# Kernel tuning notes

Measured on AMD Instinct MI355X. Metric: run time of the kernel, lower is better.

Reference implementation:

```python
import jax, jax.numpy as jnp
import numpy as np

B, N, IN_DIM, OUT_DIM = 8, 2048, 128, 128
NEG_SLOPE = 0.2

def setup_inputs() -> dict:
    key = jax.random.key(0)
    k1, k2, k3, k4 = jax.random.split(key, 4)
    x = jax.random.normal(k1, (B, N, IN_DIM), dtype=jnp.float32)
    adj = jax.random.randint(k2, (N, N), 0, 2, dtype=jnp.int32)
    # nn.Linear weight init scale ~ 1/sqrt(fan_in)
    W = jax.random.normal(k3, (IN_DIM, OUT_DIM), dtype=jnp.float32) / np.sqrt(IN_DIM)
    a_vec = jax.random.normal(k4, (2 * OUT_DIM,), dtype=jnp.float32) / np.sqrt(2 * OUT_DIM)
    return {"x": x, "adj": adj, "W": W, "a_vec": a_vec}

def reference(x, adj, W, a_vec):
    # h = x @ W : [b, n, d]
    h = jnp.einsum("bni,io->bno", x, W)
    # Algebraic decomposition of a([h_i, h_j]) = a1.h_i + a2.h_j
    a1, a2 = a_vec[:OUT_DIM], a_vec[OUT_DIM:]
    s_i = h @ a1  # [b, n] score contribution from source node i
    s_j = h @ a2  # [b, n] score contribution from target node j
    e = s_i[:, :, None] + s_j[:, None, :]  # [b, n, n]
    e = jnp.where(e >= 0, e, NEG_SLOPE * e)  # leaky_relu(0.2)
    mask = (adj > 0)[None, :, :]  # [1, n, n] broadcast over batch
    e = jnp.where(mask, e, -jnp.inf)
    alpha = jax.nn.softmax(e, axis=-1)  # [b, n, n]
    out = jnp.einsum("bnm,bmd->bnd", alpha, h)  # [b, n, d]
    return out, alpha
```

## Files before the change

kernel.cpp:

```cpp
#include <hip/hip_runtime.h>
#include <hip/hip_bf16.h>
#include <cstdint>
#include <cstddef>

constexpr int Bn = 8;
constexpr int Nn = 2048;
constexpr int Dn = 128;

typedef __bf16 bf16x8 __attribute__((ext_vector_type(8)));
typedef float f32x4 __attribute__((ext_vector_type(4)));

#define AS1 __attribute__((address_space(1)))
#define AS3 __attribute__((address_space(3)))

static __device__ __forceinline__ void gl_lds16(const void* g, void* l) {
  __builtin_amdgcn_global_load_lds((AS1 const void*)g, (AS3 void*)l, 16, 0, 0);
}

__global__ __launch_bounds__(256) void gat_k1(
    const float* __restrict__ x, const float* __restrict__ W,
    const float* __restrict__ a_vec,
    __bf16* __restrict__ hT, float* __restrict__ s1, float* __restrict__ s2) {
  __shared__ __align__(16) float Wl[64 * 144];
  __shared__ __align__(16) float xL[32 * 132];

  const int t = threadIdx.x;
  const int r0 = blockIdx.x * 32;
  const int b = r0 >> 11;
  const int n0 = r0 & (Nn - 1);
  const int rp = (t >> 4) << 1;
  const int c0 = (t & 15) << 3;
  const int c0p = c0 + ((c0 >> 5) << 2);

  float acc[2][8];
#pragma unroll
  for (int r = 0; r < 2; ++r)
#pragma unroll
    for (int c = 0; c < 8; ++c) acc[r][c] = 0.f;

#pragma unroll
  for (int it = 0; it < 4; ++it) {
    int idx = t + (it << 8);
    int rr = idx >> 5, kc = (idx & 31) << 2;
    *(float4*)(xL + rr * 132 + kc) = *(const float4*)(x + (size_t)(r0 + rr) * Dn + kc);
  }

  for (int ph = 0; ph < 2; ++ph) {
    if (ph) __syncthreads();
#pragma unroll
    for (int it = 0; it < 8; ++it) {
      int idx = t + (it << 8);
      int kk = idx >> 5, c4 = (idx & 31) << 2;
      int dsto = kk * 144 + c4 + ((c4 >> 5) << 2);
      *(float4*)(Wl + dsto) = *(const float4*)(W + (size_t)((ph << 6) + kk) * Dn + c4);
    }
    __syncthreads();
    const float* xrow = xL + rp * 132 + (ph << 6);
    for (int k = 0; k < 64; ++k) {
      float xa0 = xrow[k];
      float xa1 = xrow[132 + k];
      float4 w0 = *(const float4*)(Wl + k * 144 + c0p);
      float4 w1 = *(const float4*)(Wl + k * 144 + c0p + 4);
      float ws[8] = {w0.x, w0.y, w0.z, w0.w, w1.x, w1.y, w1.z, w1.w};
#pragma unroll
      for (int c = 0; c < 8; ++c) {
        acc[0][c] = fmaf(xa0, ws[c], acc[0][c]);
        acc[1][c] = fmaf(xa1, ws[c], acc[1][c]);
      }
    }
  }

  float q1[2] = {0.f, 0.f}, q2[2] = {0.f, 0.f};
#pragma unroll
  for (int c = 0; c < 8; ++c) {
    float a1c = a_vec[c0 + c];
    float a2c = a_vec[Dn + c0 + c];
    q1[0] = fmaf(acc[0][c], a1c, q1[0]);
    q1[1] = fmaf(acc[1][c], a1c, q1[1]);
    q2[0] = fmaf(acc[0][c], a2c, q2[0]);
    q2[1] = fmaf(acc[1][c], a2c, q2[1]);
  }
#pragma unroll
  for (int d = 1; d < 16; d <<= 1) {
    q1[0] += __shfl_xor(q1[0], d);
    q1[1] += __shfl_xor(q1[1], d);
    q2[0] += __shfl_xor(q2[0], d);
    q2[1] += __shfl_xor(q2[1], d);
  }
  if ((t & 15) == 0) {
    s1[b * Nn + n0 + rp] = q1[0];
    s1[b * Nn + n0 + rp + 1] = q1[1];
    s2[b * Nn + n0 + rp] = q2[0];
    s2[b * Nn + n0 + rp + 1] = q2[1];
  }

#pragma unroll
  for (int c = 0; c < 8; ++c) {
    union { __bf16 h[2]; uint32_t u; } pk;
    pk.h[0] = (__bf16)acc[0][c];
    pk.h[1] = (__bf16)acc[1][c];
    *(uint32_t*)(hT + (size_t)(b * Dn + c0 + c) * Nn + n0 + rp) = pk.u;
  }
}

__global__ __launch_bounds__(512) void gat_k2(
    const int* __restrict__ adj, const __bf16* __restrict__ hT,
    const float* __restrict__ s1, const float* __restrict__ s2,
    float* __restrict__ out, float* __restrict__ alpha) {
  __shared__ __align__(16) float sj[Nn];
  __shared__ float siv[32], invl[32];
  __shared__ __align__(16) __bf16 Pl[2][32 * 72];
  __shared__ __align__(16) __bf16 hl[3 * 128 * 64];

  const int t = threadIdx.x;
  const int b = blockIdx.x >> 6;
  const int i0 = (blockIdx.x & 63) << 5;
  const int w = t >> 6, lane = t & 63;
  const int ii = t >> 4, sub = t & 15;
  const int lrow = lane >> 3, ccs = lane & 7;
  const __bf16* __restrict__ hTb = hT + (size_t)b * Dn * Nn;

#pragma unroll
  for (int inst = 0; inst < 2; ++inst) {
    int row = (w << 4) + (inst << 3) + lrow;
    gl_lds16(hTb + (size_t)row * Nn + ((ccs ^ lrow) << 3),
             &hl[((w << 4) + (inst << 3)) << 6]);
  }

  *(float4*)(sj + (t << 2)) = *(const float4*)(s2 + b * Nn + (t << 2));
  if (t < 32) siv[t] = s1[b * Nn + i0 + t];
  __syncthreads();

  const int i = i0 + ii;
  const int* __restrict__ adjrow = adj + (size_t)i * Nn;
  const float si = siv[ii];

  float l = 0.f;
  uint32_t mb0 = 0, mb1 = 0, mb2 = 0, mb3 = 0;
#define PASS1_G(G, MW)                                                        \
  {                                                                           \
    _Pragma("unroll")                                                         \
    for (int u = 0; u < 8; ++u) {                                             \
      int j = (((G) << 3) + u) * 64 + (sub << 2);                             \
      int4 am = *(const int4*)(adjrow + j);                                   \
      float4 sv = *(const float4*)(sj + j);                                   \
      float e0 = si + sv.x; e0 = fmaxf(e0, 0.2f * e0);                        \
      float e1 = si + sv.y; e1 = fmaxf(e1, 0.2f * e1);                        \
      float e2 = si + sv.z; e2 = fmaxf(e2, 0.2f * e2);                        \
      float e3 = si + sv.w; e3 = fmaxf(e3, 0.2f * e3);                        \
      l += (am.x > 0) ? __expf(e0) : 0.f;                                     \
      l += (am.y > 0) ? __expf(e1) : 0.f;                                     \
      l += (am.z > 0) ? __expf(e2) : 0.f;                                     \
      l += (am.w > 0) ? __expf(e3) : 0.f;                                     \
      uint32_t mbt = (am.x > 0 ? 1u : 0u) | (am.y > 0 ? 2u : 0u) |            \
                     (am.z > 0 ? 4u : 0u) | (am.w > 0 ? 8u : 0u);             \
      MW |= mbt << (u << 2);                                                  \
    }                                                                         \
  }
  PASS1_G(0, mb0)
  PASS1_G(1, mb1)
  PASS1_G(2, mb2)
  PASS1_G(3, mb3)
#undef PASS1_G

  l += __shfl_xor(l, 1);
  l += __shfl_xor(l, 2);
  l += __shfl_xor(l, 4);
  l += __shfl_xor(l, 8);
  if (sub == 0) invl[ii] = 1.f / l;
  __syncthreads();
  const float il = invl[ii];

  const int iw = (w & 1) << 4;
  const int nd0 = (w >> 1) << 5;
  const int q16 = lane >> 4, m16 = lane & 15;
  f32x4 acc0 = {0.f, 0.f, 0.f, 0.f}, acc1 = {0.f, 0.f, 0.f, 0.f};
  float* __restrict__ arow = alpha + ((size_t)(b * Nn + i) << 11);

  auto alpha_phase = [&](int k, int parity) {
    int j = (k << 6) + (sub << 2);
    float4 sv = *(const float4*)(sj + j);
    uint32_t mw = (k & 16) ? ((k & 8) ? mb3 : mb2) : ((k & 8) ? mb1 : mb0);
    int sh = (k & 7) << 2;
    float e0 = si + sv.x; e0 = fmaxf(e0, 0.2f * e0);
    float e1 = si + sv.y; e1 = fmaxf(e1, 0.2f * e1);
    float e2 = si + sv.z; e2 = fmaxf(e2, 0.2f * e2);
    float e3 = si + sv.w; e3 = fmaxf(e3, 0.2f * e3);
    float a0 = ((mw >> (sh + 0)) & 1u) ? __expf(e0) * il : 0.f;
    float a1 = ((mw >> (sh + 1)) & 1u) ? __expf(e1) * il : 0.f;
    float a2 = ((mw >> (sh + 2)) & 1u) ? __expf(e2) * il : 0.f;
    float a3 = ((mw >> (sh + 3)) & 1u) ? __expf(e3) * il : 0.f;
    f32x4 av = {a0, a1, a2, a3};
    __builtin_nontemporal_store(av, (f32x4*)(arow + j));
    union { __bf16 h[4]; uint2 u2; } pk;
    pk.h[0] = (__bf16)a0; pk.h[1] = (__bf16)a1;
    pk.h[2] = (__bf16)a2; pk.h[3] = (__bf16)a3;
    *(uint2*)(&Pl[parity][ii * 72 + (sub << 2)]) = pk.u2;
  };

  auto mfma_phase = [&](int parity, const __bf16* hb) {
#pragma unroll
    for (int ks = 0; ks < 2; ++ks) {
      bf16x8 af = *(const bf16x8*)(&Pl[parity][(iw + m16) * 72 + (ks << 5) + (q16 << 3)]);
      {
        int d = nd0 + m16;
        int phys = ((ks << 2) + q16) ^ (d & 7);
        bf16x8 bv = *(const bf16x8*)(&hb[(d << 6) + (phys << 3)]);
        acc0 = __builtin_amdgcn_mfma_f32_16x16x32_bf16(af, bv, acc0, 0, 0, 0);
      }
      {
        int d = nd0 + 16 + m16;
        int phys = ((ks << 2) + q16) ^ (d & 7);
        bf16x8 bv = *(const bf16x8*)(&hb[(d << 6) + (phys << 3)]);
        acc1 = __builtin_amdgcn_mfma_f32_16x16x32_bf16(af, bv, acc1, 0, 0, 0);
      }
    }
  };

  auto stage = [&](int jn, int bidx) {
#pragma unroll
    for (int inst = 0; inst < 2; ++inst) {
      int row = (w << 4) + (inst << 3) + lrow;
      gl_lds16(hTb + (size_t)row * Nn + jn + ((ccs ^ lrow) << 3),
               &hl[(bidx << 13) + (((w << 4) + (inst << 3)) << 6)]);
    }
  };

  stage(64, 1);
  __builtin_amdgcn_sched_barrier(0);
  alpha_phase(0, 0);
  asm volatile("s_waitcnt lgkmcnt(0)\n\ts_barrier" ::: "memory");

  int bi = 0;
  for (int jt = 0; jt < 30; ++jt) {
    int bp = bi + 2;
    if (bp >= 3) bp -= 3;
    stage((jt + 2) << 6, bp);
    __builtin_amdgcn_sched_barrier(0);
    mfma_phase(jt & 1, &hl[bi << 13]);
    alpha_phase(jt + 1, (jt + 1) & 1);
    asm volatile("s_waitcnt vmcnt(4) lgkmcnt(0)\n\ts_barrier" ::: "memory");
    bi = (bi == 2) ? 0 : bi + 1;
  }
  mfma_phase(0, &hl[0]);
  alpha_phase(31, 1);
  asm volatile("s_waitcnt vmcnt(2) lgkmcnt(0)\n\ts_barrier" ::: "memory");
  mfma_phase(1, &hl[1 << 13]);

#pragma unroll
  for (int nb = 0; nb < 2; ++nb) {
    f32x4 a = nb ? acc1 : acc0;
    int d = nd0 + (nb << 4) + m16;
#pragma unroll
    for (int r = 0; r < 4; ++r) {
      int irow = i0 + iw + (q16 << 2) + r;
      out[((size_t)(b * Nn + irow) << 7) + d] = a[r];
    }
  }
}

extern "C" void kernel_launch(void* const* d_in, const int* in_sizes, int n_in,
                              void* d_out, int out_size, void* d_ws, size_t ws_size,
                              hipStream_t stream) {
  const float* x = (const float*)d_in[0];
  const int* adj = (const int*)d_in[1];
  const float* W = (const float*)d_in[2];
  const float* a_vec = (const float*)d_in[3];

  float* out = (float*)d_out;
  float* alpha = out + (size_t)Bn * Nn * Dn;

  char* ws = (char*)d_ws;
  __bf16* hT = (__bf16*)ws;
  float* s1 = (float*)(ws + (size_t)Bn * Dn * Nn * 2);
  float* s2 = s1 + (size_t)Bn * Nn;

  gat_k1<<<512, 256, 0, stream>>>(x, W, a_vec, hT, s1, s2);
  gat_k2<<<512, 512, 0, stream>>>(adj, hT, s1, s2, out, alpha);
}
```

Measured before the change: 213.4 us.

## Load hT B-operands directly from global into registers, drop LDS triple buffer

```diff
diff --git a/kernel.cpp b/kernel.cpp
--- a/kernel.cpp
+++ b/kernel.cpp
@@ -9,13 +9,6 @@
 
 typedef __bf16 bf16x8 __attribute__((ext_vector_type(8)));
 typedef float f32x4 __attribute__((ext_vector_type(4)));
-
-#define AS1 __attribute__((address_space(1)))
-#define AS3 __attribute__((address_space(3)))
-
-static __device__ __forceinline__ void gl_lds16(const void* g, void* l) {
-  __builtin_amdgcn_global_load_lds((AS1 const void*)g, (AS3 void*)l, 16, 0, 0);
-}
 
 __global__ __launch_bounds__(256) void gat_k1(
     const float* __restrict__ x, const float* __restrict__ W,
@@ -110,22 +103,15 @@
   __shared__ __align__(16) float sj[Nn];
   __shared__ float siv[32], invl[32];
   __shared__ __align__(16) __bf16 Pl[2][32 * 72];
-  __shared__ __align__(16) __bf16 hl[3 * 128 * 64];
 
   const int t = threadIdx.x;
   const int b = blockIdx.x >> 6;
   const int i0 = (blockIdx.x & 63) << 5;
   const int w = t >> 6, lane = t & 63;
   const int ii = t >> 4, sub = t & 15;
-  const int lrow = lane >> 3, ccs = lane & 7;
+  const int q16 = lane >> 4, m16 = lane & 15;
+  const int d0 = w << 4;
   const __bf16* __restrict__ hTb = hT + (size_t)b * Dn * Nn;
-
-#pragma unroll
-  for (int inst = 0; inst < 2; ++inst) {
-    int row = (w << 4) + (inst << 3) + lrow;
-    gl_lds16(hTb + (size_t)row * Nn + ((ccs ^ lrow) << 3),
-             &hl[((w << 4) + (inst << 3)) << 6]);
-  }
 
   *(float4*)(sj + (t << 2)) = *(const float4*)(s2 + b * Nn + (t << 2));
   if (t < 32) siv[t] = s1[b * Nn + i0 + t];
@@ -171,13 +157,12 @@
   __syncthreads();
   const float il = invl[ii];
 
-  const int iw = (w & 1) << 4;
-  const int nd0 = (w >> 1) << 5;
-  const int q16 = lane >> 4, m16 = lane & 15;
   f32x4 acc0 = {0.f, 0.f, 0.f, 0.f}, acc1 = {0.f, 0.f, 0.f, 0.f};
   float* __restrict__ arow = alpha + ((size_t)(b * Nn + i) << 11);
 
-  auto alpha_phase = [&](int k, int parity) {
+  const __bf16* __restrict__ bp = hTb + (size_t)(d0 + m16) * Nn + (q16 << 3);
+
+  auto alpha_phase = [&](int k) {
     int j = (k << 6) + (sub << 2);
     float4 sv = *(const float4*)(sj + j);
     uint32_t mw = (k & 16) ? ((k & 8) ? mb3 : mb2) : ((k & 8) ? mb1 : mb0);
@@ -195,65 +180,45 @@
     union { __bf16 h[4]; uint2 u2; } pk;
     pk.h[0] = (__bf16)a0; pk.h[1] = (__bf16)a1;
     pk.h[2] = (__bf16)a2; pk.h[3] = (__bf16)a3;
-    *(uint2*)(&Pl[parity][ii * 72 + (sub << 2)]) = pk.u2;
+    *(uint2*)(&Pl[k & 1][ii * 72 + (sub << 2)]) = pk.u2;
   };
 
-  auto mfma_phase = [&](int parity, const __bf16* hb) {
-#pragma unroll
-    for (int ks = 0; ks < 2; ++ks) {
-      bf16x8 af = *(const bf16x8*)(&Pl[parity][(iw + m16) * 72 + (ks << 5) + (q16 << 3)]);
-      {
-        int d = nd0 + m16;
-        int phys = ((ks << 2) + q16) ^ (d & 7);
-        bf16x8 bv = *(const bf16x8*)(&hb[(d << 6) + (phys << 3)]);
-        acc0 = __builtin_amdgcn_mfma_f32_16x16x32_bf16(af, bv, acc0, 0, 0, 0);
-      }
-      {
-        int d = nd0 + 16 + m16;
-        int phys = ((ks << 2) + q16) ^ (d & 7);
-        bf16x8 bv = *(const bf16x8*)(&hb[(d << 6) + (phys << 3)]);
-        acc1 = __builtin_amdgcn_mfma_f32_16x16x32_bf16(af, bv, acc1, 0, 0, 0);
-      }
-    }
+  auto mfma_win = [&](int k, bf16x8 bc0, bf16x8 bc1) {
+    const __bf16* plb = Pl[k & 1];
+    bf16x8 a00 = *(const bf16x8*)(plb + m16 * 72 + (q16 << 3));
+    bf16x8 a01 = *(const bf16x8*)(plb + m16 * 72 + 32 + (q16 << 3));
+    bf16x8 a10 = *(const bf16x8*)(plb + (16 + m16) * 72 + (q16 << 3));
+    bf16x8 a11 = *(const bf16x8*)(plb + (16 + m16) * 72 + 32 + (q16 << 3));
+    acc0 = __builtin_amdgcn_mfma_f32_16x16x32_bf16(a00, bc0, acc0, 0, 0, 0);
+    acc0 = __builtin_amdgcn_mfma_f32_16x16x32_bf16(a01, bc1, acc0, 0, 0, 0);
+    acc1 = __builtin_amdgcn_mfma_f32_16x16x32_bf16(a10, bc0, acc1, 0, 0, 0);
+    acc1 = __builtin_amdgcn_mfma_f32_16x16x32_bf16(a11, bc1, acc1, 0, 0, 0);
   };
 
-  auto stage = [&](int jn, int bidx) {
-#pragma unroll
-    for (int inst = 0; inst < 2; ++inst) {
-      int row = (w << 4) + (inst << 3) + lrow;
-      gl_lds16(hTb + (size_t)row * Nn + jn + ((ccs ^ lrow) << 3),
-               &hl[(bidx << 13) + (((w << 4) + (inst << 3)) << 6)]);
-    }
-  };
-
-  stage(64, 1);
-  __builtin_amdgcn_sched_barrier(0);
-  alpha_phase(0, 0);
+  bf16x8 c0 = *(const bf16x8*)(bp);
+  bf16x8 c1 = *(const bf16x8*)(bp + 32);
+  alpha_phase(0);
   asm volatile("s_waitcnt lgkmcnt(0)\n\ts_barrier" ::: "memory");
 
-  int bi = 0;
-  for (int jt = 0; jt < 30; ++jt) {
-    int bp = bi + 2;
-    if (bp >= 3) bp -= 3;
-    stage((jt + 2) << 6, bp);
+#pragma unroll
+  for (int jt = 0; jt < 31; ++jt) {
+    bf16x8 n0 = *(const bf16x8*)(bp + ((jt + 1) << 6));
+    bf16x8 n1 = *(const bf16x8*)(bp + ((jt + 1) << 6) + 32);
     __builtin_amdgcn_sched_barrier(0);
-    mfma_phase(jt & 1, &hl[bi << 13]);
-    alpha_phase(jt + 1, (jt + 1) & 1);
-    asm volatile("s_waitcnt vmcnt(4) lgkmcnt(0)\n\ts_barrier" ::: "memory");
-    bi = (bi == 2) ? 0 : bi + 1;
-  }
-  mfma_phase(0, &hl[0]);
-  alpha_phase(31, 1);
-  asm volatile("s_waitcnt vmcnt(2) lgkmcnt(0)\n\ts_barrier" ::: "memory");
-  mfma_phase(1, &hl[1 << 13]);
-
-#pragma unroll
-  for (int nb = 0; nb < 2; ++nb) {
-    f32x4 a = nb ? acc1 : acc0;
-    int d = nd0 + (nb << 4) + m16;
+    mfma_win(jt, c0, c1);
+    alpha_phase(jt + 1);
+    asm volatile("s_waitcnt lgkmcnt(0)\n\ts_barrier" ::: "memory");
+    c0 = n0; c1 = n1;
+  }
+  mfma_win(31, c0, c1);
+
+#pragma unroll
+  for (int ib = 0; ib < 2; ++ib) {
+    f32x4 a = ib ? acc1 : acc0;
+    int d = d0 + m16;
 #pragma unroll
     for (int r = 0; r < 4; ++r) {
-      int irow = i0 + iw + (q16 << 2) + r;
+      int irow = i0 + (ib << 4) + (q16 << 2) + r;
       out[((size_t)(b * Nn + irow) << 7) + d] = a[r];
     }
   }
```

New measurement: 196.3 us. 1.09x faster.
